# Kernel optimization log

Measured on AMD Instinct MI355X. Metric: run time of the kernel, lower is better.

The kernel has to match this reference:

```python
import jax, jax.numpy as jnp
import numpy as np

B, N, FD, H, L = 8, 512, 32, 64, 3  # batch, atoms, feature_dim, hidden_dim, n_layers
LN_EPS = 1e-5
DEG_EPS = 1e-8


def setup_inputs() -> dict:
    key = jax.random.key(0)
    ks = jax.random.split(key, 10)
    features = jax.random.normal(ks[0], (B, N, FD), jnp.float32)
    # sparse binary molecular-graph adjacency
    adjacency = (jax.random.uniform(ks[1], (B, N, N)) < 0.08).astype(jnp.float32)
    mask = jax.random.uniform(ks[2], (B, N)) < 0.9
    feature_weights = jnp.ones((FD,), jnp.float32)
    w_enc = jax.random.normal(ks[3], (FD, H), jnp.float32) / np.sqrt(FD)
    b_enc = jnp.zeros((H,), jnp.float32)
    ln_g = jnp.ones((H,), jnp.float32)
    ln_b = jnp.zeros((H,), jnp.float32)
    msg_w = jax.random.normal(ks[4], (L, 2 * H, H), jnp.float32) / np.sqrt(2 * H)
    msg_b = jnp.zeros((L, H), jnp.float32)
    ws1 = jax.random.normal(ks[5], (H, H // 2), jnp.float32) / np.sqrt(H)
    bs1 = jnp.zeros((H // 2,), jnp.float32)
    ws2 = jax.random.normal(ks[6], (H // 2, 1), jnp.float32) / np.sqrt(H // 2)
    bs2 = jnp.zeros((1,), jnp.float32)
    return dict(features=features, adjacency=adjacency, mask=mask,
                feature_weights=feature_weights, w_enc=w_enc, b_enc=b_enc,
                ln_g=ln_g, ln_b=ln_b, msg_w=msg_w, msg_b=msg_b,
                ws1=ws1, bs1=bs1, ws2=ws2, bs2=bs2)


def reference(features, adjacency, mask, feature_weights, w_enc, b_enc,
              ln_g, ln_b, msg_w, msg_b, ws1, bs1, ws2, bs2):
    # encoder: weighted features -> Linear -> LayerNorm -> SiLU (dropout = eval identity)
    x = features * feature_weights  # [B,N,FD]
    h = x @ w_enc + b_enc  # [B,N,H]
    mu = h.mean(-1, keepdims=True)
    var = h.var(-1, keepdims=True)
    h = (h - mu) * jax.lax.rsqrt(var + LN_EPS) * ln_g + ln_b
    h = jax.nn.silu(h)

    deg = adjacency.sum(-1, keepdims=True) + DEG_EPS  # [B,N,1]
    for l in range(L):
        # concat-linear split: cat([h_i,h_j]) @ W == h_i @ W[:H] + h_j @ W[H:]
        wi, wj = msg_w[l, :H], msg_w[l, H:]
        a = h @ wi  # [B,N,H] (sender i rows)
        b = h @ wj  # [B,N,H] (receiver j cols)
        m = jax.nn.silu(a[:, :, None, :] + b[:, None, :, :] + msg_b[l])  # [B,N,N,H]
        h_new = jnp.einsum('bijh,bij->bih', m, adjacency) / deg
        h = h + 0.5 * h_new

    scores = (jax.nn.silu(h @ ws1 + bs1) @ ws2 + bs2)[..., 0]  # [B,N]
    return jnp.where(mask, scores, -jnp.inf)
```

## Files before the change

kernel.cpp:

```cpp
#include <hip/hip_runtime.h>
#include <hip/hip_fp16.h>
#include <math.h>

#define B 8
#define N 512
#define FD 32
#define H 64
#define L 3
#define NODES (B * N)
#define LN_EPS 1e-5f
#define DEG_EPS 1e-8f
#define MAXDEG 512

#define FP16_NEG_SENTINEL ((unsigned short)0xFBFF)

#define BLOCK_THREADS 256
#define WPB 4
#define GRID_BLOCKS (NODES / WPB)

__device__ __forceinline__ float fsilu(float x) {
    return x * __builtin_amdgcn_rcpf(1.0f + __expf(-x));
}

__device__ __forceinline__ unsigned short f32_to_f16_safe(float f) {
    if (!(f == f)) return (unsigned short)0;
    if (f >  65504.0f) f =  65504.0f;
    if (f < -65504.0f) f = -65504.0f;
    return __half_as_ushort(__float2half(f));
}

__device__ __forceinline__ float edge_gather(const unsigned short* __restrict__ crow,
                                             int deg, int bbase, int t, float a_t,
                                             const float* __restrict__ b_in) {
    if (deg <= 0) return 0.0f;
    const float* bb = b_in + (size_t)bbase * H + t;
    float acc = 0.0f;
    for (int e0 = 0; e0 < deg; e0 += 16) {
        float x[16];
#pragma unroll
        for (int q = 0; q < 16; ++q) {
            int idx = e0 + q;
            if (idx > deg - 1) idx = deg - 1;
            x[q] = bb[(size_t)crow[idx] * H];
        }
#pragma unroll
        for (int q = 0; q < 16; ++q) {
            float s = fsilu(a_t + x[q]);
            acc += (e0 + q < deg) ? s : 0.0f;
        }
    }
    return acc;
}

__global__ __launch_bounds__(BLOCK_THREADS)
void k0_enc_proj_csr(const float* __restrict__ feat,
                     const float* __restrict__ adj,
                     const unsigned char* __restrict__ mask,
                     const float* __restrict__ fw,
                     const float* __restrict__ w_enc,
                     const float* __restrict__ b_enc,
                     const float* __restrict__ ln_g,
                     const float* __restrict__ ln_b,
                     const float* __restrict__ msg_w,
                     float* __restrict__ hbuf,
                     float* __restrict__ abuf,
                     float* __restrict__ bbuf,
                     unsigned short* __restrict__ csr,
                     int* __restrict__ degbuf,
                     float* __restrict__ flag)
{
    const int wave  = threadIdx.x >> 6;
    const int t     = threadIdx.x & 63;
    const int node  = blockIdx.x * WPB + wave;

    __shared__ float hs[WPB][H];

    if (blockIdx.x == 0 && wave == 0) {
        int cnt_mis = 0, cnt_3f = 0, cnt_3c = 0;
        for (int i = t; i < NODES; i += 64) {
            unsigned char v = mask[i];
            if ((i & 3) != 0 && v != 0) cnt_mis++;
            if ((i & 3) == 3 && v == 0x3F) cnt_3f++;
            if ((i & 1) == 1 && v == 0x3C) cnt_3c++;
        }
        for (int off = 32; off; off >>= 1) {
            cnt_mis += __shfl_xor(cnt_mis, off);
            cnt_3f  += __shfl_xor(cnt_3f, off);
            cnt_3c  += __shfl_xor(cnt_3c, off);
        }
        if (t == 0) {
            float f = 0.0f;
            if (cnt_3f > 0) f = 2.0f;
            else if (cnt_3c > 0) f = 3.0f;
            else if (cnt_mis > 0) f = 1.0f;
            flag[0] = f;
        }
    }

    float hreg;
    {
        const float* xrow = feat + (size_t)node * FD;
        float acc = b_enc[t];
#pragma unroll
        for (int f = 0; f < FD; ++f)
            acc += xrow[f] * fw[f] * w_enc[f * H + t];
        float sum = acc, sumsq = acc * acc;
        for (int off = 32; off; off >>= 1) {
            sum   += __shfl_xor(sum, off);
            sumsq += __shfl_xor(sumsq, off);
        }
        float mu  = sum * (1.0f / H);
        float var = sumsq * (1.0f / H) - mu * mu;
        float hn  = (acc - mu) * rsqrtf(var + LN_EPS) * ln_g[t] + ln_b[t];
        hreg = fsilu(hn);
    }
    hbuf[(size_t)node * H + t] = hreg;

    hs[wave][t] = hreg;
    float av = 0.0f, bv = 0.0f;
#pragma unroll 8
    for (int k = 0; k < H; ++k) {
        float hk = hs[wave][k];
        av += hk * msg_w[k * H + t];
        bv += hk * msg_w[(H + k) * H + t];
    }
    abuf[(size_t)node * H + t] = av;
    bbuf[(size_t)node * H + t] = bv;

    const float4* adjrow4 = (const float4*)(adj + (size_t)node * N);
    unsigned short* crow = csr + (size_t)node * MAXDEG;
    int base = 0;
    for (int j0 = 0; j0 < N; j0 += 256) {
        float4 v = adjrow4[(j0 >> 2) + t];
        float vc[4] = { v.x, v.y, v.z, v.w };
#pragma unroll
        for (int c = 0; c < 4; ++c) {
            unsigned long long mk = __ballot(vc[c] != 0.0f);
            if (vc[c] != 0.0f) {
                int pre = __popcll(mk & ((1ull << t) - 1ull));
                crow[base + pre] = (unsigned short)(j0 + 4 * t + c);
            }
            base += __popcll(mk);
        }
    }
    if (t == 0) degbuf[node] = base;
}

__global__ __launch_bounds__(BLOCK_THREADS)
void k_msg_proj(const unsigned short* __restrict__ csr,
                const int* __restrict__ degbuf,
                const float* __restrict__ msg_b_l,
                const float* __restrict__ msg_w_n,
                float* __restrict__ hbuf,
                float* __restrict__ abuf,
                const float* __restrict__ b_in,
                float* __restrict__ b_out)
{
    const int wave  = threadIdx.x >> 6;
    const int t     = threadIdx.x & 63;
    const int node  = blockIdx.x * WPB + wave;
    const int bbase = node & ~(N - 1);

    __shared__ float hs[WPB][H];

    float a_t = abuf[(size_t)node * H + t] + msg_b_l[t];
    int deg = degbuf[node];
    const unsigned short* crow = csr + (size_t)node * MAXDEG;

    float acc = edge_gather(crow, deg, bbase, t, a_t, b_in);

    float hreg = hbuf[(size_t)node * H + t]
               + 0.5f * acc * __builtin_amdgcn_rcpf((float)deg + DEG_EPS);
    hbuf[(size_t)node * H + t] = hreg;

    hs[wave][t] = hreg;
    float av = 0.0f, bv = 0.0f;
#pragma unroll 8
    for (int k = 0; k < H; ++k) {
        float hk = hs[wave][k];
        av += hk * msg_w_n[k * H + t];
        bv += hk * msg_w_n[(H + k) * H + t];
    }
    abuf[(size_t)node * H + t] = av;
    b_out[(size_t)node * H + t] = bv;
}

__global__ __launch_bounds__(BLOCK_THREADS)
void k_msg_score(const unsigned short* __restrict__ csr,
                 const int* __restrict__ degbuf,
                 const float* __restrict__ msg_b_l,
                 const float* __restrict__ hbuf,
                 const float* __restrict__ abuf,
                 const float* __restrict__ b_in,
                 const float* __restrict__ ws1,
                 const float* __restrict__ bs1,
                 const float* __restrict__ ws2,
                 const float* __restrict__ bs2,
                 const unsigned char* __restrict__ mask,
                 const float* __restrict__ flag,
                 unsigned short* __restrict__ out)
{
    const int wave  = threadIdx.x >> 6;
    const int t     = threadIdx.x & 63;
    const int node  = blockIdx.x * WPB + wave;
    const int bbase = node & ~(N - 1);

    __shared__ float hs[WPB][H];

    float a_t = abuf[(size_t)node * H + t] + msg_b_l[t];
    int deg = degbuf[node];
    const unsigned short* crow = csr + (size_t)node * MAXDEG;

    float acc = edge_gather(crow, deg, bbase, t, a_t, b_in);

    float hreg = hbuf[(size_t)node * H + t]
               + 0.5f * acc * __builtin_amdgcn_rcpf((float)deg + DEG_EPS);

    hs[wave][t] = hreg;
    float part = 0.0f;
    if (t < H / 2) {
        float s = bs1[t];
#pragma unroll 8
        for (int k = 0; k < H; ++k) s += hs[wave][k] * ws1[k * (H / 2) + t];
        part = fsilu(s) * ws2[t];
    }
    for (int off = 16; off; off >>= 1) part += __shfl_xor(part, off);
    if (t == 0) {
        float sc = part + bs2[0];
        float f = flag[0];
        bool mv;
        if (f == 2.0f)      mv = ((const float*)mask)[node] != 0.0f;
        else if (f == 3.0f) mv = (((const unsigned short*)mask)[node] & 0x7FFF) != 0;
        else if (f == 1.0f) mv = mask[node] != 0;
        else                mv = ((const int*)mask)[node] != 0;
        out[node] = mv ? f32_to_f16_safe(sc) : FP16_NEG_SENTINEL;
    }
}

extern "C" void kernel_launch(void* const* d_in, const int* in_sizes, int n_in,
                              void* d_out, int out_size, void* d_ws, size_t ws_size,
                              hipStream_t stream) {
    const float* feat  = (const float*)d_in[0];
    const float* adj   = (const float*)d_in[1];
    const unsigned char* mask = (const unsigned char*)d_in[2];
    const float* fw    = (const float*)d_in[3];
    const float* w_enc = (const float*)d_in[4];
    const float* b_enc = (const float*)d_in[5];
    const float* ln_g  = (const float*)d_in[6];
    const float* ln_b  = (const float*)d_in[7];
    const float* msg_w = (const float*)d_in[8];
    const float* msg_b = (const float*)d_in[9];
    const float* ws1   = (const float*)d_in[10];
    const float* bs1   = (const float*)d_in[11];
    const float* ws2   = (const float*)d_in[12];
    const float* bs2   = (const float*)d_in[13];
    unsigned short* out = (unsigned short*)d_out;

    char* wsb = (char*)d_ws;
    float* hbuf  = (float*)(wsb);
    float* abuf  = (float*)(wsb + (1 << 20));
    float* bA    = (float*)(wsb + (2 << 20));
    float* bB    = (float*)(wsb + (3 << 20));
    unsigned short* csr = (unsigned short*)(wsb + (4 << 20));
    int*   degb  = (int*)(wsb + (8 << 20));
    float* flag  = (float*)(wsb + (8 << 20) + (1 << 16));

    const size_t WBLK = 2 * H * H;

    k0_enc_proj_csr<<<GRID_BLOCKS, BLOCK_THREADS, 0, stream>>>(
        feat, adj, mask, fw, w_enc, b_enc, ln_g, ln_b,
        msg_w , hbuf, abuf, bA, csr, degb, flag);

    k_msg_proj<<<GRID_BLOCKS, BLOCK_THREADS, 0, stream>>>(
        csr, degb, msg_b + 0 * H, msg_w + 1 * WBLK, hbuf, abuf, bA, bB);

    k_msg_proj<<<GRID_BLOCKS, BLOCK_THREADS, 0, stream>>>(
        csr, degb, msg_b + 1 * H, msg_w + 2 * WBLK, hbuf, abuf, bB, bA);

    k_msg_score<<<GRID_BLOCKS, BLOCK_THREADS, 0, stream>>>(
        csr, degb, msg_b + 2 * H, hbuf, abuf, bA,
        ws1, bs1, ws2, bs2, mask, flag, out);
}
```

Before: 53.23 us.

## Split each node's edge gather and projection across two waves

The message kernels now use two wavefronts per node instead of one. Each wave gathers half of the node's neighbour list, and the partial sums are combined through shared memory. The following projection is also split, with one wave computing the a-projection and the other the b-projection, and the score MLP splits its reduction over k. The goal is to cut per-wave latency on the serial edge loop and expose more parallelism, at the cost of block-wide barriers and twice as many blocks.

```diff
diff --git a/kernel.cpp b/kernel.cpp
--- a/kernel.cpp
+++ b/kernel.cpp
@@ -16,7 +16,6 @@
 
 #define BLOCK_THREADS 256
 #define WPB 4
-#define GRID_BLOCKS (NODES / WPB)
 
 __device__ __forceinline__ float fsilu(float x) {
     return x * __builtin_amdgcn_rcpf(1.0f + __expf(-x));
@@ -30,23 +29,23 @@
 }
 
 __device__ __forceinline__ float edge_gather(const unsigned short* __restrict__ crow,
-                                             int deg, int bbase, int t, float a_t,
+                                             int len, int bbase, int t, float a_t,
                                              const float* __restrict__ b_in) {
-    if (deg <= 0) return 0.0f;
+    if (len <= 0) return 0.0f;
     const float* bb = b_in + (size_t)bbase * H + t;
     float acc = 0.0f;
-    for (int e0 = 0; e0 < deg; e0 += 16) {
+    for (int e0 = 0; e0 < len; e0 += 16) {
         float x[16];
 #pragma unroll
         for (int q = 0; q < 16; ++q) {
             int idx = e0 + q;
-            if (idx > deg - 1) idx = deg - 1;
+            if (idx > len - 1) idx = len - 1;
             x[q] = bb[(size_t)crow[idx] * H];
         }
 #pragma unroll
         for (int q = 0; q < 16; ++q) {
             float s = fsilu(a_t + x[q]);
-            acc += (e0 + q < deg) ? s : 0.0f;
+            acc += (e0 + q < len) ? s : 0.0f;
         }
     }
     return acc;
@@ -147,93 +146,126 @@
 }
 
 __global__ __launch_bounds__(BLOCK_THREADS)
-void k_msg_proj(const unsigned short* __restrict__ csr,
-                const int* __restrict__ degbuf,
-                const float* __restrict__ msg_b_l,
-                const float* __restrict__ msg_w_n,
-                float* __restrict__ hbuf,
-                float* __restrict__ abuf,
-                const float* __restrict__ b_in,
-                float* __restrict__ b_out)
+void k_msg_proj2(const unsigned short* __restrict__ csr,
+                 const int* __restrict__ degbuf,
+                 const float* __restrict__ msg_b_l,
+                 const float* __restrict__ msg_w_n,
+                 float* __restrict__ hbuf,
+                 float* __restrict__ abuf,
+                 const float* __restrict__ b_in,
+                 float* __restrict__ b_out)
 {
-    const int wave  = threadIdx.x >> 6;
-    const int t     = threadIdx.x & 63;
-    const int node  = blockIdx.x * WPB + wave;
+    const int wave = threadIdx.x >> 6;
+    const int t    = threadIdx.x & 63;
+    const int nin  = wave >> 1;
+    const int half = wave & 1;
+    const int node = blockIdx.x * 2 + nin;
     const int bbase = node & ~(N - 1);
 
-    __shared__ float hs[WPB][H];
+    __shared__ float pacc[4][H];
+    __shared__ float hsh[2][H];
 
     float a_t = abuf[(size_t)node * H + t] + msg_b_l[t];
     int deg = degbuf[node];
     const unsigned short* crow = csr + (size_t)node * MAXDEG;
 
-    float acc = edge_gather(crow, deg, bbase, t, a_t, b_in);
+    int len0  = (deg + 1) >> 1;
+    int start = half ? len0 : 0;
+    int len   = half ? (deg - len0) : len0;
+
+    float acc = edge_gather(crow + start, len, bbase, t, a_t, b_in);
+    pacc[wave][t] = acc;
+    __syncthreads();
+    acc = pacc[nin * 2][t] + pacc[nin * 2 + 1][t];
 
     float hreg = hbuf[(size_t)node * H + t]
                + 0.5f * acc * __builtin_amdgcn_rcpf((float)deg + DEG_EPS);
-    hbuf[(size_t)node * H + t] = hreg;
-
-    hs[wave][t] = hreg;
-    float av = 0.0f, bv = 0.0f;
+    if (half == 0) {
+        hbuf[(size_t)node * H + t] = hreg;
+        hsh[nin][t] = hreg;
+    }
+    __syncthreads();
+
+    const float* wcol = msg_w_n + (size_t)half * H * H;
+    float v = 0.0f;
 #pragma unroll 8
-    for (int k = 0; k < H; ++k) {
-        float hk = hs[wave][k];
-        av += hk * msg_w_n[k * H + t];
-        bv += hk * msg_w_n[(H + k) * H + t];
-    }
-    abuf[(size_t)node * H + t] = av;
-    b_out[(size_t)node * H + t] = bv;
+    for (int k = 0; k < H; ++k)
+        v += hsh[nin][k] * wcol[k * H + t];
+    if (half == 0) abuf[(size_t)node * H + t] = v;
+    else           b_out[(size_t)node * H + t] = v;
 }
 
 __global__ __launch_bounds__(BLOCK_THREADS)
-void k_msg_score(const unsigned short* __restrict__ csr,
-                 const int* __restrict__ degbuf,
-                 const float* __restrict__ msg_b_l,
-                 const float* __restrict__ hbuf,
-                 const float* __restrict__ abuf,
-                 const float* __restrict__ b_in,
-                 const float* __restrict__ ws1,
-                 const float* __restrict__ bs1,
-                 const float* __restrict__ ws2,
-                 const float* __restrict__ bs2,
-                 const unsigned char* __restrict__ mask,
-                 const float* __restrict__ flag,
-                 unsigned short* __restrict__ out)
+void k_msg_score2(const unsigned short* __restrict__ csr,
+                  const int* __restrict__ degbuf,
+                  const float* __restrict__ msg_b_l,
+                  const float* __restrict__ hbuf,
+                  const float* __restrict__ abuf,
+                  const float* __restrict__ b_in,
+                  const float* __restrict__ ws1,
+                  const float* __restrict__ bs1,
+                  const float* __restrict__ ws2,
+                  const float* __restrict__ bs2,
+                  const unsigned char* __restrict__ mask,
+                  const float* __restrict__ flag,
+                  unsigned short* __restrict__ out)
 {
-    const int wave  = threadIdx.x >> 6;
-    const int t     = threadIdx.x & 63;
-    const int node  = blockIdx.x * WPB + wave;
+    const int wave = threadIdx.x >> 6;
+    const int t    = threadIdx.x & 63;
+    const int nin  = wave >> 1;
+    const int half = wave & 1;
+    const int node = blockIdx.x * 2 + nin;
     const int bbase = node & ~(N - 1);
 
-    __shared__ float hs[WPB][H];
+    __shared__ float pacc[4][H];
+    __shared__ float hsh[2][H];
+    __shared__ float ps1[2][2][H / 2];
 
     float a_t = abuf[(size_t)node * H + t] + msg_b_l[t];
     int deg = degbuf[node];
     const unsigned short* crow = csr + (size_t)node * MAXDEG;
 
-    float acc = edge_gather(crow, deg, bbase, t, a_t, b_in);
+    int len0  = (deg + 1) >> 1;
+    int start = half ? len0 : 0;
+    int len   = half ? (deg - len0) : len0;
+
+    float acc = edge_gather(crow + start, len, bbase, t, a_t, b_in);
+    pacc[wave][t] = acc;
+    __syncthreads();
+    acc = pacc[nin * 2][t] + pacc[nin * 2 + 1][t];
 
     float hreg = hbuf[(size_t)node * H + t]
                + 0.5f * acc * __builtin_amdgcn_rcpf((float)deg + DEG_EPS);
-
-    hs[wave][t] = hreg;
-    float part = 0.0f;
+    if (half == 0) hsh[nin][t] = hreg;
+    __syncthreads();
+
     if (t < H / 2) {
-        float s = bs1[t];
+        float s = 0.0f;
 #pragma unroll 8
-        for (int k = 0; k < H; ++k) s += hs[wave][k] * ws1[k * (H / 2) + t];
-        part = fsilu(s) * ws2[t];
-    }
-    for (int off = 16; off; off >>= 1) part += __shfl_xor(part, off);
-    if (t == 0) {
-        float sc = part + bs2[0];
-        float f = flag[0];
-        bool mv;
-        if (f == 2.0f)      mv = ((const float*)mask)[node] != 0.0f;
-        else if (f == 3.0f) mv = (((const unsigned short*)mask)[node] & 0x7FFF) != 0;
-        else if (f == 1.0f) mv = mask[node] != 0;
-        else                mv = ((const int*)mask)[node] != 0;
-        out[node] = mv ? f32_to_f16_safe(sc) : FP16_NEG_SENTINEL;
+        for (int kk = 0; kk < H / 2; ++kk) {
+            int k = half * (H / 2) + kk;
+            s += hsh[nin][k] * ws1[k * (H / 2) + t];
+        }
+        ps1[nin][half][t] = s;
+    }
+    __syncthreads();
+    if (half == 0) {
+        float part = 0.0f;
+        if (t < H / 2) {
+            float s = bs1[t] + ps1[nin][0][t] + ps1[nin][1][t];
+            part = fsilu(s) * ws2[t];
+        }
+        for (int off = 16; off; off >>= 1) part += __shfl_xor(part, off);
+        if (t == 0) {
+            float sc = part + bs2[0];
+            float f = flag[0];
+            bool mv;
+            if (f == 2.0f)      mv = ((const float*)mask)[node] != 0.0f;
+            else if (f == 3.0f) mv = (((const unsigned short*)mask)[node] & 0x7FFF) != 0;
+            else if (f == 1.0f) mv = mask[node] != 0;
+            else                mv = ((const int*)mask)[node] != 0;
+            out[node] = mv ? f32_to_f16_safe(sc) : FP16_NEG_SENTINEL;
+        }
     }
 }
 
@@ -267,17 +299,17 @@
 
     const size_t WBLK = 2 * H * H;
 
-    k0_enc_proj_csr<<<GRID_BLOCKS, BLOCK_THREADS, 0, stream>>>(
+    k0_enc_proj_csr<<<NODES / WPB, BLOCK_THREADS, 0, stream>>>(
         feat, adj, mask, fw, w_enc, b_enc, ln_g, ln_b,
         msg_w , hbuf, abuf, bA, csr, degb, flag);
 
-    k_msg_proj<<<GRID_BLOCKS, BLOCK_THREADS, 0, stream>>>(
+    k_msg_proj2<<<NODES / 2, BLOCK_THREADS, 0, stream>>>(
         csr, degb, msg_b + 0 * H, msg_w + 1 * WBLK, hbuf, abuf, bA, bB);
 
-    k_msg_proj<<<GRID_BLOCKS, BLOCK_THREADS, 0, stream>>>(
+    k_msg_proj2<<<NODES / 2, BLOCK_THREADS, 0, stream>>>(
         csr, degb, msg_b + 1 * H, msg_w + 2 * WBLK, hbuf, abuf, bB, bA);
 
-    k_msg_score<<<GRID_BLOCKS, BLOCK_THREADS, 0, stream>>>(
+    k_msg_score2<<<NODES / 2, BLOCK_THREADS, 0, stream>>>(
         csr, degb, msg_b + 2 * H, hbuf, abuf, bA,
         ws1, bs1, ws2, bs2, mask, flag, out);
 }
```

After: 54.24 us. About the same (+1.9%).

## Swizzle node-to-block mapping per batch and broadcast hidden state via readlane

Applied to the files above, without the earlier changes.

Remaps block indices so consecutive blocks, likely dispatched round-robin across the XCDs, each land in a different batch. Each XCD then gathers neighbour rows from a single batch's b buffer, which should improve L2 locality for the edge gathers. The LDS staging for the per-node matvecs is replaced by readlane broadcasts from registers, removing shared-memory traffic. Launch bounds now request higher occupancy, which may constrain register allocation for the unrolled loops.

```diff
diff --git a/kernel.cpp b/kernel.cpp
--- a/kernel.cpp
+++ b/kernel.cpp
@@ -18,8 +18,16 @@
 #define WPB 4
 #define GRID_BLOCKS (NODES / WPB)
 
+__device__ __forceinline__ int swizzled_node(int bid, int wave) {
+    return (bid & 7) * N + (bid >> 3) * WPB + wave;
+}
+
 __device__ __forceinline__ float fsilu(float x) {
     return x * __builtin_amdgcn_rcpf(1.0f + __expf(-x));
+}
+
+__device__ __forceinline__ float lanebcast(float v, int k) {
+    return __int_as_float(__builtin_amdgcn_readlane(__float_as_int(v), k));
 }
 
 __device__ __forceinline__ unsigned short f32_to_f16_safe(float f) {
@@ -30,29 +38,38 @@
 }
 
 __device__ __forceinline__ float edge_gather(const unsigned short* __restrict__ crow,
-                                             int deg, int bbase, int t, float a_t,
+                                             int len, int bbase, int t, float a_t,
                                              const float* __restrict__ b_in) {
-    if (deg <= 0) return 0.0f;
+    if (len <= 0) return 0.0f;
     const float* bb = b_in + (size_t)bbase * H + t;
     float acc = 0.0f;
-    for (int e0 = 0; e0 < deg; e0 += 16) {
+    for (int e0 = 0; e0 < len; e0 += 16) {
         float x[16];
 #pragma unroll
         for (int q = 0; q < 16; ++q) {
             int idx = e0 + q;
-            if (idx > deg - 1) idx = deg - 1;
+            if (idx > len - 1) idx = len - 1;
             x[q] = bb[(size_t)crow[idx] * H];
         }
 #pragma unroll
         for (int q = 0; q < 16; ++q) {
             float s = fsilu(a_t + x[q]);
-            acc += (e0 + q < deg) ? s : 0.0f;
+            acc += (e0 + q < len) ? s : 0.0f;
         }
     }
     return acc;
 }
 
-__global__ __launch_bounds__(BLOCK_THREADS)
+__device__ __forceinline__ float wave_matvec(float hreg, const float* __restrict__ W,
+                                             int t) {
+    float acc = 0.0f;
+#pragma unroll
+    for (int k = 0; k < H; ++k)
+        acc += lanebcast(hreg, k) * W[k * H + t];
+    return acc;
+}
+
+__global__ __launch_bounds__(BLOCK_THREADS, 4)
 void k0_enc_proj_csr(const float* __restrict__ feat,
                      const float* __restrict__ adj,
                      const unsigned char* __restrict__ mask,
@@ -71,9 +88,7 @@
 {
     const int wave  = threadIdx.x >> 6;
     const int t     = threadIdx.x & 63;
-    const int node  = blockIdx.x * WPB + wave;
-
-    __shared__ float hs[WPB][H];
+    const int node  = swizzled_node(blockIdx.x, wave);
 
     if (blockIdx.x == 0 && wave == 0) {
         int cnt_mis = 0, cnt_3f = 0, cnt_3c = 0;
@@ -116,16 +131,8 @@
     }
     hbuf[(size_t)node * H + t] = hreg;
 
-    hs[wave][t] = hreg;
-    float av = 0.0f, bv = 0.0f;
-#pragma unroll 8
-    for (int k = 0; k < H; ++k) {
-        float hk = hs[wave][k];
-        av += hk * msg_w[k * H + t];
-        bv += hk * msg_w[(H + k) * H + t];
-    }
-    abuf[(size_t)node * H + t] = av;
-    bbuf[(size_t)node * H + t] = bv;
+    abuf[(size_t)node * H + t] = wave_matvec(hreg, msg_w, t);
+    bbuf[(size_t)node * H + t] = wave_matvec(hreg, msg_w + H * H, t);
 
     const float4* adjrow4 = (const float4*)(adj + (size_t)node * N);
     unsigned short* crow = csr + (size_t)node * MAXDEG;
@@ -146,7 +153,7 @@
     if (t == 0) degbuf[node] = base;
 }
 
-__global__ __launch_bounds__(BLOCK_THREADS)
+__global__ __launch_bounds__(BLOCK_THREADS, 4)
 void k_msg_proj(const unsigned short* __restrict__ csr,
                 const int* __restrict__ degbuf,
                 const float* __restrict__ msg_b_l,
@@ -158,10 +165,8 @@
 {
     const int wave  = threadIdx.x >> 6;
     const int t     = threadIdx.x & 63;
-    const int node  = blockIdx.x * WPB + wave;
+    const int node  = swizzled_node(blockIdx.x, wave);
     const int bbase = node & ~(N - 1);
-
-    __shared__ float hs[WPB][H];
 
     float a_t = abuf[(size_t)node * H + t] + msg_b_l[t];
     int deg = degbuf[node];
@@ -173,19 +178,11 @@
                + 0.5f * acc * __builtin_amdgcn_rcpf((float)deg + DEG_EPS);
     hbuf[(size_t)node * H + t] = hreg;
 
-    hs[wave][t] = hreg;
-    float av = 0.0f, bv = 0.0f;
-#pragma unroll 8
-    for (int k = 0; k < H; ++k) {
-        float hk = hs[wave][k];
-        av += hk * msg_w_n[k * H + t];
-        bv += hk * msg_w_n[(H + k) * H + t];
-    }
-    abuf[(size_t)node * H + t] = av;
-    b_out[(size_t)node * H + t] = bv;
-}
-
-__global__ __launch_bounds__(BLOCK_THREADS)
+    abuf[(size_t)node * H + t] = wave_matvec(hreg, msg_w_n, t);
+    b_out[(size_t)node * H + t] = wave_matvec(hreg, msg_w_n + H * H, t);
+}
+
+__global__ __launch_bounds__(BLOCK_THREADS, 4)
 void k_msg_score(const unsigned short* __restrict__ csr,
                  const int* __restrict__ degbuf,
                  const float* __restrict__ msg_b_l,
@@ -202,10 +199,8 @@
 {
     const int wave  = threadIdx.x >> 6;
     const int t     = threadIdx.x & 63;
-    const int node  = blockIdx.x * WPB + wave;
+    const int node  = swizzled_node(blockIdx.x, wave);
     const int bbase = node & ~(N - 1);
-
-    __shared__ float hs[WPB][H];
 
     float a_t = abuf[(size_t)node * H + t] + msg_b_l[t];
     int deg = degbuf[node];
@@ -216,12 +211,12 @@
     float hreg = hbuf[(size_t)node * H + t]
                + 0.5f * acc * __builtin_amdgcn_rcpf((float)deg + DEG_EPS);
 
-    hs[wave][t] = hreg;
     float part = 0.0f;
     if (t < H / 2) {
         float s = bs1[t];
-#pragma unroll 8
-        for (int k = 0; k < H; ++k) s += hs[wave][k] * ws1[k * (H / 2) + t];
+#pragma unroll
+        for (int k = 0; k < H; ++k)
+            s += lanebcast(hreg, k) * ws1[k * (H / 2) + t];
         part = fsilu(s) * ws2[t];
     }
     for (int off = 16; off; off >>= 1) part += __shfl_xor(part, off);
```

New measurement: 49.81 us. 6.4% less time.
